# Optimization experiments

Measured on AMD Instinct MI355X. Metric: run time of the kernel, lower is better.

Reference implementation:

```python
import jax, jax.numpy as jnp
import numpy as np

N = 50000          # node_num
E = 800000         # edges before self-loops (avg degree 16)
H = 1              # heads
C = 64             # out_channel (== embedding dim)
D_IN = 64          # in_channel
NEG_SLOPE = 0.2    # GraphLayer leaky_relu negative_slope
BN_EPS = 1e-5


def setup_inputs() -> dict:
    key = jax.random.key(0)
    ks = jax.random.split(key, 12)
    x = jax.random.normal(ks[0], (N, D_IN), jnp.float32)
    # random edges with no self-loops (forward removes then re-adds self-loops)
    src = jax.random.randint(ks[1], (E,), 0, N, dtype=jnp.int32)
    off = jax.random.randint(ks[2], (E,), 1, N, dtype=jnp.int32)
    dst = (src + off) % N
    edge_index = jnp.stack([src, dst])            # [2, E], row0=j (source), row1=i (target)
    embedding = jax.random.normal(ks[3], (N, C), jnp.float32)
    sc = 1.0 / np.sqrt(D_IN)
    W = jax.random.normal(ks[4], (H * C, D_IN), jnp.float32) * sc   # lin.weight
    att_i = jax.random.normal(ks[5], (1, H, C), jnp.float32) * 0.1
    att_j = jax.random.normal(ks[6], (1, H, C), jnp.float32) * 0.1
    att_em_i = jax.random.normal(ks[7], (1, H, C), jnp.float32) * 0.1
    att_em_j = jax.random.normal(ks[8], (1, H, C), jnp.float32) * 0.1
    bias = jnp.zeros((C,), jnp.float32)           # GraphLayer bias (concat=False)
    bn_gamma = jnp.ones((C,), jnp.float32)
    bn_beta = jnp.zeros((C,), jnp.float32)
    return {"x": x, "edge_index": edge_index, "embedding": embedding, "W": W,
            "att_i": att_i, "att_j": att_j, "att_em_i": att_em_i, "att_em_j": att_em_j,
            "bias": bias, "bn_gamma": bn_gamma, "bn_beta": bn_beta}


def reference(x, edge_index, embedding, W, att_i, att_j, att_em_i, att_em_j, bias, bn_gamma, bn_beta):
    n = x.shape[0]
    xl = (x @ W.T).reshape(n, H, C)                       # lin(x) -> [N, H, C]
    # add self-loops (input edges have none)
    loops = jnp.arange(n, dtype=edge_index.dtype)
    src = jnp.concatenate([edge_index[0], loops])         # j
    dst = jnp.concatenate([edge_index[1], loops])         # i (aggregation target)
    x_j = xl[src]                                         # [E', H, C]
    x_i = xl[dst]
    emb_i = embedding[dst][:, None, :]                    # [E', 1, C] broadcast over heads
    emb_j = embedding[src][:, None, :]
    # alpha = <cat(x_i, emb_i), cat(att_i, att_em_i)> + <cat(x_j, emb_j), cat(att_j, att_em_j)>
    a = ((x_i * att_i).sum(-1) + (emb_i * att_em_i).sum(-1)
         + (x_j * att_j).sum(-1) + (emb_j * att_em_j).sum(-1))   # [E', H]
    a = jnp.where(a >= 0, a, NEG_SLOPE * a)               # leaky_relu(0.2)
    # segment softmax over target nodes
    amax = jax.ops.segment_max(a, dst, num_segments=n)    # every node has a self-loop
    ea = jnp.exp(a - amax[dst])
    denom = jax.ops.segment_sum(ea, dst, num_segments=n)
    alpha = ea / (denom[dst] + 1e-16)                     # [E', H]
    msg = x_j * alpha[..., None]                          # [E', H, C]
    out = jax.ops.segment_sum(msg, dst, num_segments=n)   # [N, H, C]
    out = out.mean(axis=1) + bias                         # concat=False -> head mean
    # BatchNorm1d (training mode: batch stats) + ReLU
    mu = out.mean(axis=0)
    var = ((out - mu) ** 2).mean(axis=0)
    out = (out - mu) * jax.lax.rsqrt(var + BN_EPS) * bn_gamma + bn_beta
    return jnp.maximum(out, 0.0)
```

## Files before the change

kernel.cpp:

```cpp
#include <hip/hip_runtime.h>
#include <hip/hip_bf16.h>

#define NEG_SLOPE 0.2f
#define BN_EPS 1e-5f
#define CAP 48
#define OWNMAX 768

typedef __attribute__((ext_vector_type(8))) short bf16x8;
typedef __attribute__((ext_vector_type(4))) float f32x4;

__device__ __forceinline__ bf16x8 pk8(float4 a, float4 b) {
    union { __hip_bfloat16 h; short s; } u;
    bf16x8 r;
    u.h = __float2bfloat16(a.x); r[0] = u.s;
    u.h = __float2bfloat16(a.y); r[1] = u.s;
    u.h = __float2bfloat16(a.z); r[2] = u.s;
    u.h = __float2bfloat16(a.w); r[3] = u.s;
    u.h = __float2bfloat16(b.x); r[4] = u.s;
    u.h = __float2bfloat16(b.y); r[5] = u.s;
    u.h = __float2bfloat16(b.z); r[6] = u.s;
    u.h = __float2bfloat16(b.w); r[7] = u.s;
    return r;
}

__global__ void __launch_bounds__(256, 8)
k_scatter_mfma(const float* __restrict__ x, const float* __restrict__ W,
               const float* __restrict__ emb,
               const float* __restrict__ att_i, const float* __restrict__ att_j,
               const float* __restrict__ att_em_i, const float* __restrict__ att_em_j,
               const int* __restrict__ src, const int* __restrict__ dst, int E,
               int* __restrict__ cursor, unsigned short* __restrict__ bucket,
               __hip_bfloat16* __restrict__ xlh, float* __restrict__ s_i,
               float* __restrict__ s_j, int N) {
    __shared__ int nown;
    __shared__ int ownidx[OWNMAX];
    __shared__ int owndst[OWNMAX];
    int tid = threadIdx.x;
    {
        int myx = blockIdx.x & 7;
        int slice = blockIdx.x >> 3;
        int per = ((E + 255) >> 8);
        per = (per + 3) & ~3;
        int e0 = slice * per;
        int e1 = e0 + per; if (e1 > E) e1 = E;
        if (tid == 0) nown = 0;
        __syncthreads();
        if (e0 < e1) {
            int e1a = e0 + ((e1 - e0) & ~3);
#define APP(dd, ee) if ((((dd) >> 6) & 7) == myx) { \
            int k_ = atomicAdd(&nown, 1); \
            if (k_ < OWNMAX) { ownidx[k_] = (ee); owndst[k_] = (dd); } }
            for (int e = e0 + tid * 4; e < e1a; e += 1024) {
                int4 d4 = *(const int4*)(dst + e);
                APP(d4.x, e)
                APP(d4.y, e + 1)
                APP(d4.z, e + 2)
                APP(d4.w, e + 3)
            }
            for (int e = e1a + tid; e < e1; e += 256) {
                int d = dst[e];
                APP(d, e)
            }
#undef APP
        }
        __syncthreads();
        int n = nown < OWNMAX ? nown : OWNMAX;
        int k0 = tid, k1 = tid + 256;
        bool v0 = k0 < n, v1 = k1 < n;
        int ea = v0 ? ownidx[k0] : 0, da = v0 ? owndst[k0] : 0;
        int eb = v1 ? ownidx[k1] : 0, db = v1 ? owndst[k1] : 0;
        int sa = v0 ? src[ea] : 0;
        int sb = v1 ? src[eb] : 0;
        if (v0) {
            int p = atomicAdd(&cursor[da], 1);
            if (p < CAP) bucket[(size_t)da * CAP + p] = (unsigned short)sa;
        }
        if (v1) {
            int p = atomicAdd(&cursor[db], 1);
            if (p < CAP) bucket[(size_t)db * CAP + p] = (unsigned short)sb;
        }
        for (int k = tid + 512; k < n; k += 256) {
            int e = ownidx[k];
            int d = owndst[k];
            int p = atomicAdd(&cursor[d], 1);
            if (p < CAP) bucket[(size_t)d * CAP + p] = (unsigned short)src[e];
        }
    }

    int gw = blockIdx.x * 4 + (tid >> 6);
    int ntiles = (N + 15) >> 4;
    if (gw >= ntiles) return;
    int lane = tid & 63;
    int m = lane & 15;
    int q = lane >> 4;
    int r0 = gw * 16;

    const float* xrow = x + (size_t)(r0 + m) * 64;
    float4 xa0 = *(const float4*)(xrow + q * 8);
    float4 xa1 = *(const float4*)(xrow + q * 8 + 4);
    float4 xb0 = *(const float4*)(xrow + 32 + q * 8);
    float4 xb1 = *(const float4*)(xrow + 32 + q * 8 + 4);
    bf16x8 A0 = pk8(xa0, xa1);
    bf16x8 A1 = pk8(xb0, xb1);

    f32x4 acc0 = {0.f, 0.f, 0.f, 0.f}, acc1 = acc0, acc2 = acc0, acc3 = acc0;
#define CTILE(ct, accv) { \
        const float* wrow = W + (size_t)(ct * 16 + m) * 64; \
        float4 wb0 = *(const float4*)(wrow + q * 8); \
        float4 wb1 = *(const float4*)(wrow + q * 8 + 4); \
        float4 wb2 = *(const float4*)(wrow + 32 + q * 8); \
        float4 wb3 = *(const float4*)(wrow + 32 + q * 8 + 4); \
        bf16x8 B0 = pk8(wb0, wb1); \
        bf16x8 B1 = pk8(wb2, wb3); \
        accv = __builtin_amdgcn_mfma_f32_16x16x32_bf16(A0, B0, accv, 0, 0, 0); \
        accv = __builtin_amdgcn_mfma_f32_16x16x32_bf16(A1, B1, accv, 0, 0, 0); }
    CTILE(0, acc0) CTILE(1, acc1) CTILE(2, acc2) CTILE(3, acc3)
#undef CTILE

    float ati0 = att_i[m],    ati1 = att_i[16 + m],    ati2 = att_i[32 + m],    ati3 = att_i[48 + m];
    float atj0 = att_j[m],    atj1 = att_j[16 + m],    atj2 = att_j[32 + m],    atj3 = att_j[48 + m];
    float aei0 = att_em_i[m], aei1 = att_em_i[16 + m], aei2 = att_em_i[32 + m], aei3 = att_em_i[48 + m];
    float aej0 = att_em_j[m], aej1 = att_em_j[16 + m], aej2 = att_em_j[32 + m], aej3 = att_em_j[48 + m];
#pragma unroll
    for (int reg = 0; reg < 4; ++reg) {
        int r = r0 + q * 4 + reg;
        if (r < N) {
            float v0 = acc0[reg], v1 = acc1[reg], v2 = acc2[reg], v3 = acc3[reg];
            __hip_bfloat16* xo = xlh + (size_t)r * 64 + m;
            xo[0]  = __float2bfloat16(v0);
            xo[16] = __float2bfloat16(v1);
            xo[32] = __float2bfloat16(v2);
            xo[48] = __float2bfloat16(v3);
            const float* er = emb + (size_t)r * 64 + m;
            float e0 = er[0], e1 = er[16], e2 = er[32], e3 = er[48];
            float pi = v0 * ati0 + v1 * ati1 + v2 * ati2 + v3 * ati3
                     + e0 * aei0 + e1 * aei1 + e2 * aei2 + e3 * aei3;
            float pj = v0 * atj0 + v1 * atj1 + v2 * atj2 + v3 * atj3
                     + e0 * aej0 + e1 * aej1 + e2 * aej2 + e3 * aej3;
#pragma unroll
            for (int o = 1; o < 16; o <<= 1) {
                pi += __shfl_xor(pi, o, 64);
                pj += __shfl_xor(pj, o, 64);
            }
            if (m == 0) { s_i[r] = pi; s_j[r] = pj; }
        }
    }
}

__global__ void __launch_bounds__(256, 8)
k_aggregate(const __hip_bfloat16* __restrict__ xlh, const float* __restrict__ s_i,
            const float* __restrict__ s_j, const int* __restrict__ cursor,
            const unsigned short* __restrict__ bucket, const float* __restrict__ bias,
            __hip_bfloat16* __restrict__ preh, int N) {
    int lane = threadIdx.x & 63;
    int w = threadIdx.x >> 6;
    int blk = blockIdx.x;
    int t = blk >> 3;
    int g = ((t >> 4) << 7) + ((blk & 7) << 4) + (t & 15);
    int i = g * 4 + w;
    if (i >= N) return;

    int deg = cursor[i];
    deg = deg < CAP ? deg : CAP;
    size_t base = (size_t)i * CAP;
    float sii = s_i[i];
    float sji = s_j[i];
    float selfx = (float)xlh[(size_t)i * 64 + lane];
    float bi = bias[lane];
    int jreg = 0;
    if (lane < deg) jreg = (int)bucket[base + lane];
    float areg = -1e30f;
    if (lane < deg) {
        float a = sii + s_j[jreg];
        areg = a >= 0.f ? a : NEG_SLOPE * a;
    }
    float a_self = sii + sji;
    a_self = a_self >= 0.f ? a_self : NEG_SLOPE * a_self;
    float mx = fmaxf(a_self, areg);
#pragma unroll
    for (int o = 32; o; o >>= 1) mx = fmaxf(mx, __shfl_xor(mx, o, 64));
    float wreg = (lane < deg) ? __expf(areg - mx) : 0.f;
    float dsum = wreg;
#pragma unroll
    for (int o = 32; o; o >>= 1) dsum += __shfl_xor(dsum, o, 64);
    float w_self = __expf(a_self - mx);
    float denom = dsum + w_self + 1e-16f;

    float acc = w_self * selfx;
    int wbits = __float_as_int(wreg);
    int nb = (deg + 15) >> 4;
#define GL(k) int j##k = __builtin_amdgcn_readlane(jreg, e + k); \
              float u##k = __int_as_float(__builtin_amdgcn_readlane(wbits, e + k)); \
              float v##k = (float)xlh[(size_t)j##k * 64 + lane];
#define FM(k) acc = fmaf(u##k, v##k, acc);
    for (int b = 0; b < nb; ++b) {
        int e = b << 4;
        GL(0) GL(1) GL(2) GL(3) GL(4) GL(5) GL(6) GL(7)
        GL(8) GL(9) GL(10) GL(11) GL(12) GL(13) GL(14) GL(15)
        FM(0) FM(1) FM(2) FM(3) FM(4) FM(5) FM(6) FM(7)
        FM(8) FM(9) FM(10) FM(11) FM(12) FM(13) FM(14) FM(15)
    }
#undef GL
#undef FM
    preh[(size_t)i * 64 + lane] = __float2bfloat16(acc / denom + bi);
}

__global__ void k_stats(const __hip_bfloat16* __restrict__ preh, int N,
                        float* __restrict__ sums) {
    int lane = threadIdx.x & 63, w = threadIdx.x >> 6;
    int gwave = blockIdx.x * (blockDim.x >> 6) + w;
    int stride = gridDim.x * (blockDim.x >> 6);
    float s = 0.f, q = 0.f;
    for (int r = gwave; r < N; r += stride) {
        float v = (float)preh[(size_t)r * 64 + lane];
        s += v;
        q = fmaf(v, v, q);
    }
    __shared__ float ls[4][64], lq[4][64];
    ls[w][lane] = s;
    lq[w][lane] = q;
    __syncthreads();
    if (w == 0) {
        s = ls[0][lane] + ls[1][lane] + ls[2][lane] + ls[3][lane];
        q = lq[0][lane] + lq[1][lane] + lq[2][lane] + lq[3][lane];
        atomicAdd(&sums[lane], s);
        atomicAdd(&sums[64 + lane], q);
    }
}

__global__ void __launch_bounds__(256, 4)
k_norm(const __hip_bfloat16* __restrict__ preh, const float* __restrict__ sums,
       const float* __restrict__ gamma, const float* __restrict__ beta,
       float* __restrict__ out, int N, int total4) {
    __shared__ float sc_sh[64], sh_sh[64];
    int tid = threadIdx.x;
    if (tid < 64) {
        float invN = 1.f / (float)N;
        float mu = sums[tid] * invN;
        float var = sums[64 + tid] * invN - mu * mu;
        float sc = gamma[tid] * rsqrtf(var + BN_EPS);
        sc_sh[tid] = sc;
        sh_sh[tid] = beta[tid] - mu * sc;
    }
    __syncthreads();
    typedef __attribute__((ext_vector_type(4))) short s16x4;
    union { s16x4 v; short s[4]; } u;
    for (int i = blockIdx.x * blockDim.x + tid; i < total4; i += gridDim.x * blockDim.x) {
        int c = (i & 15) * 4;
        u.v = ((const s16x4*)preh)[i];
        float4 r;
        union { __hip_bfloat16 h; short s; } cv;
        cv.s = u.s[0]; r.x = fmaxf(fmaf((float)cv.h, sc_sh[c + 0], sh_sh[c + 0]), 0.f);
        cv.s = u.s[1]; r.y = fmaxf(fmaf((float)cv.h, sc_sh[c + 1], sh_sh[c + 1]), 0.f);
        cv.s = u.s[2]; r.z = fmaxf(fmaf((float)cv.h, sc_sh[c + 2], sh_sh[c + 2]), 0.f);
        cv.s = u.s[3]; r.w = fmaxf(fmaf((float)cv.h, sc_sh[c + 3], sh_sh[c + 3]), 0.f);
        ((float4*)out)[i] = r;
    }
}

extern "C" void kernel_launch(void* const* d_in, const int* in_sizes, int n_in,
                              void* d_out, int out_size, void* d_ws, size_t ws_size,
                              hipStream_t stream) {
    const float* x        = (const float*)d_in[0];
    const int*   ei       = (const int*)d_in[1];
    const float* emb      = (const float*)d_in[2];
    const float* W        = (const float*)d_in[3];
    const float* att_i    = (const float*)d_in[4];
    const float* att_j    = (const float*)d_in[5];
    const float* att_em_i = (const float*)d_in[6];
    const float* att_em_j = (const float*)d_in[7];
    const float* bias     = (const float*)d_in[8];
    const float* gamma    = (const float*)d_in[9];
    const float* beta     = (const float*)d_in[10];

    int N = in_sizes[0] / 64;
    int E = in_sizes[1] / 2;
    const int* srcv = ei;
    const int* dstv = ei + E;

    char* ws = (char*)d_ws;
    size_t o = 0;
    auto alloc = [&](size_t bytes) -> char* {
        char* p = ws + o;
        o += bytes;
        o = (o + 255) & ~(size_t)255;
        return p;
    };
    __hip_bfloat16* xlh    = (__hip_bfloat16*)alloc((size_t)N * 64 * 2);
    __hip_bfloat16* preh   = (__hip_bfloat16*)alloc((size_t)N * 64 * 2);
    float* s_i             = (float*)alloc((size_t)N * 4);
    float* s_j             = (float*)alloc((size_t)N * 4);
    unsigned short* bucket = (unsigned short*)alloc((size_t)N * CAP * 2);
    char*  zbase  = alloc((size_t)N * 4 + 128 * 4);
    int*   cursor = (int*)zbase;
    float* sums   = (float*)(zbase + (size_t)N * 4);

    hipMemsetAsync(zbase, 0, (size_t)N * 4 + 128 * 4, stream);

    k_scatter_mfma<<<2048, 256, 0, stream>>>(x, W, emb, att_i, att_j, att_em_i,
                                             att_em_j, srcv, dstv, E, cursor, bucket,
                                             xlh, s_i, s_j, N);
    int nblk2 = (((N + 3) / 4) + 127) & ~127;
    k_aggregate<<<nblk2, 256, 0, stream>>>(xlh, s_i, s_j, cursor, bucket,
                                           bias, preh, N);
    k_stats<<<256, 256, 0, stream>>>(preh, N, sums);
    int total4 = N * 16;
    k_norm<<<512, 256, 0, stream>>>(preh, sums, gamma, beta, (float*)d_out, N, total4);
}
```

Baseline: 179.7 us.

## Fuse BN stats into aggregate, pack src/dst in LDS, hoist x loads

The scatter kernel now reads src alongside dst and packs both as 16-bit halves into one LDS word. This removes the dependent global src[e] gather in the bucket-fill phase and halves LDS usage. The x-row loads for the MFMA tile are issued before the scatter phase so their latency overlaps it. The aggregate kernel becomes a persistent grid-stride loop over a fixed 2048-block grid with XCD-aware node mapping, and it accumulates BatchNorm sums directly, which eliminates the separate k_stats kernel and its re-read of preh. The packing assumes node indices fit in 16 bits, the same assumption the existing bucket storage already makes.

Result: slower. 204.6 us (+13.9%).

```diff
diff --git a/kernel.cpp b/kernel.cpp
--- a/kernel.cpp
+++ b/kernel.cpp
@@ -33,9 +33,22 @@
                __hip_bfloat16* __restrict__ xlh, float* __restrict__ s_i,
                float* __restrict__ s_j, int N) {
     __shared__ int nown;
-    __shared__ int ownidx[OWNMAX];
-    __shared__ int owndst[OWNMAX];
+    __shared__ unsigned int own[OWNMAX];
     int tid = threadIdx.x;
+
+    int gw = blockIdx.x * 4 + (tid >> 6);
+    int ntiles = (N + 15) >> 4;
+    int lane = tid & 63;
+    int m = lane & 15;
+    int q = lane >> 4;
+    int r0 = gw * 16;
+    int rload = r0 + m; if (rload > N - 1) rload = N - 1;
+    const float* xrow = x + (size_t)rload * 64;
+    float4 xa0 = *(const float4*)(xrow + q * 8);
+    float4 xa1 = *(const float4*)(xrow + q * 8 + 4);
+    float4 xb0 = *(const float4*)(xrow + 32 + q * 8);
+    float4 xb1 = *(const float4*)(xrow + 32 + q * 8 + 4);
+
     {
         int myx = blockIdx.x & 7;
         int slice = blockIdx.x >> 3;
@@ -47,59 +60,46 @@
         __syncthreads();
         if (e0 < e1) {
             int e1a = e0 + ((e1 - e0) & ~3);
-#define APP(dd, ee) if ((((dd) >> 6) & 7) == myx) { \
+#define APP(dd, ss) if ((((dd) >> 6) & 7) == myx) { \
             int k_ = atomicAdd(&nown, 1); \
-            if (k_ < OWNMAX) { ownidx[k_] = (ee); owndst[k_] = (dd); } }
+            if (k_ < OWNMAX) own[k_] = ((unsigned)(dd) << 16) | (unsigned)(ss); }
             for (int e = e0 + tid * 4; e < e1a; e += 1024) {
                 int4 d4 = *(const int4*)(dst + e);
-                APP(d4.x, e)
-                APP(d4.y, e + 1)
-                APP(d4.z, e + 2)
-                APP(d4.w, e + 3)
+                int4 s4 = *(const int4*)(src + e);
+                APP(d4.x, s4.x)
+                APP(d4.y, s4.y)
+                APP(d4.z, s4.z)
+                APP(d4.w, s4.w)
             }
             for (int e = e1a + tid; e < e1; e += 256) {
-                int d = dst[e];
-                APP(d, e)
+                int d = dst[e]; int s = src[e];
+                APP(d, s)
             }
 #undef APP
         }
         __syncthreads();
         int n = nown < OWNMAX ? nown : OWNMAX;
-        int k0 = tid, k1 = tid + 256;
-        bool v0 = k0 < n, v1 = k1 < n;
-        int ea = v0 ? ownidx[k0] : 0, da = v0 ? owndst[k0] : 0;
-        int eb = v1 ? ownidx[k1] : 0, db = v1 ? owndst[k1] : 0;
-        int sa = v0 ? src[ea] : 0;
-        int sb = v1 ? src[eb] : 0;
-        if (v0) {
-            int p = atomicAdd(&cursor[da], 1);
-            if (p < CAP) bucket[(size_t)da * CAP + p] = (unsigned short)sa;
-        }
-        if (v1) {
-            int p = atomicAdd(&cursor[db], 1);
-            if (p < CAP) bucket[(size_t)db * CAP + p] = (unsigned short)sb;
+        unsigned pa = (tid < n) ? own[tid] : 0u;
+        unsigned pb = (tid + 256 < n) ? own[tid + 256] : 0u;
+        if (tid < n) {
+            int d = pa >> 16;
+            int p = atomicAdd(&cursor[d], 1);
+            if (p < CAP) bucket[(size_t)d * CAP + p] = (unsigned short)(pa & 0xffffu);
+        }
+        if (tid + 256 < n) {
+            int d = pb >> 16;
+            int p = atomicAdd(&cursor[d], 1);
+            if (p < CAP) bucket[(size_t)d * CAP + p] = (unsigned short)(pb & 0xffffu);
         }
         for (int k = tid + 512; k < n; k += 256) {
-            int e = ownidx[k];
-            int d = owndst[k];
+            unsigned pc = own[k];
+            int d = pc >> 16;
             int p = atomicAdd(&cursor[d], 1);
-            if (p < CAP) bucket[(size_t)d * CAP + p] = (unsigned short)src[e];
-        }
-    }
-
-    int gw = blockIdx.x * 4 + (tid >> 6);
-    int ntiles = (N + 15) >> 4;
+            if (p < CAP) bucket[(size_t)d * CAP + p] = (unsigned short)(pc & 0xffffu);
+        }
+    }
+
     if (gw >= ntiles) return;
-    int lane = tid & 63;
-    int m = lane & 15;
-    int q = lane >> 4;
-    int r0 = gw * 16;
-
-    const float* xrow = x + (size_t)(r0 + m) * 64;
-    float4 xa0 = *(const float4*)(xrow + q * 8);
-    float4 xa1 = *(const float4*)(xrow + q * 8 + 4);
-    float4 xb0 = *(const float4*)(xrow + 32 + q * 8);
-    float4 xb1 = *(const float4*)(xrow + 32 + q * 8 + 4);
     bf16x8 A0 = pk8(xa0, xa1);
     bf16x8 A1 = pk8(xb0, xb1);
 
@@ -151,80 +151,73 @@
 k_aggregate(const __hip_bfloat16* __restrict__ xlh, const float* __restrict__ s_i,
             const float* __restrict__ s_j, const int* __restrict__ cursor,
             const unsigned short* __restrict__ bucket, const float* __restrict__ bias,
-            __hip_bfloat16* __restrict__ preh, int N) {
+            __hip_bfloat16* __restrict__ preh, float* __restrict__ sums, int N) {
     int lane = threadIdx.x & 63;
     int w = threadIdx.x >> 6;
-    int blk = blockIdx.x;
-    int t = blk >> 3;
-    int g = ((t >> 4) << 7) + ((blk & 7) << 4) + (t & 15);
-    int i = g * 4 + w;
-    if (i >= N) return;
-
-    int deg = cursor[i];
-    deg = deg < CAP ? deg : CAP;
-    size_t base = (size_t)i * CAP;
-    float sii = s_i[i];
-    float sji = s_j[i];
-    float selfx = (float)xlh[(size_t)i * 64 + lane];
+    int xg = blockIdx.x & 7;
+    int t = blockIdx.x >> 3;
     float bi = bias[lane];
-    int jreg = 0;
-    if (lane < deg) jreg = (int)bucket[base + lane];
-    float areg = -1e30f;
-    if (lane < deg) {
-        float a = sii + s_j[jreg];
-        areg = a >= 0.f ? a : NEG_SLOPE * a;
-    }
-    float a_self = sii + sji;
-    a_self = a_self >= 0.f ? a_self : NEG_SLOPE * a_self;
-    float mx = fmaxf(a_self, areg);
+    float bs = 0.f, bq = 0.f;
+    int nmax = ((N + 511) >> 9) << 6;
+    for (int n = t * 4 + w; n < nmax; n += 1024) {
+        int i = ((n >> 6) << 9) | (xg << 6) | (n & 63);
+        if (i < N) {
+            int deg = cursor[i];
+            deg = deg < CAP ? deg : CAP;
+            size_t base = (size_t)i * CAP;
+            float sii = s_i[i];
+            float sji = s_j[i];
+            float selfx = (float)xlh[(size_t)i * 64 + lane];
+            int jreg = 0;
+            if (lane < deg) jreg = (int)bucket[base + lane];
+            float areg = -1e30f;
+            if (lane < deg) {
+                float a = sii + s_j[jreg];
+                areg = a >= 0.f ? a : NEG_SLOPE * a;
+            }
+            float a_self = sii + sji;
+            a_self = a_self >= 0.f ? a_self : NEG_SLOPE * a_self;
+            float mx = fmaxf(a_self, areg);
 #pragma unroll
-    for (int o = 32; o; o >>= 1) mx = fmaxf(mx, __shfl_xor(mx, o, 64));
-    float wreg = (lane < deg) ? __expf(areg - mx) : 0.f;
-    float dsum = wreg;
+            for (int o = 32; o; o >>= 1) mx = fmaxf(mx, __shfl_xor(mx, o, 64));
+            float wreg = (lane < deg) ? __expf(areg - mx) : 0.f;
+            float dsum = wreg;
 #pragma unroll
-    for (int o = 32; o; o >>= 1) dsum += __shfl_xor(dsum, o, 64);
-    float w_self = __expf(a_self - mx);
-    float denom = dsum + w_self + 1e-16f;
-
-    float acc = w_self * selfx;
-    int wbits = __float_as_int(wreg);
-    int nb = (deg + 15) >> 4;
+            for (int o = 32; o; o >>= 1) dsum += __shfl_xor(dsum, o, 64);
+            float w_self = __expf(a_self - mx);
+            float denom = dsum + w_self + 1e-16f;
+
+            float acc = w_self * selfx;
+            int wbits = __float_as_int(wreg);
+            int nb = (deg + 15) >> 4;
 #define GL(k) int j##k = __builtin_amdgcn_readlane(jreg, e + k); \
               float u##k = __int_as_float(__builtin_amdgcn_readlane(wbits, e + k)); \
               float v##k = (float)xlh[(size_t)j##k * 64 + lane];
 #define FM(k) acc = fmaf(u##k, v##k, acc);
-    for (int b = 0; b < nb; ++b) {
-        int e = b << 4;
-        GL(0) GL(1) GL(2) GL(3) GL(4) GL(5) GL(6) GL(7)
-        GL(8) GL(9) GL(10) GL(11) GL(12) GL(13) GL(14) GL(15)
-        FM(0) FM(1) FM(2) FM(3) FM(4) FM(5) FM(6) FM(7)
-        FM(8) FM(9) FM(10) FM(11) FM(12) FM(13) FM(14) FM(15)
-    }
+            for (int b = 0; b < nb; ++b) {
+                int e = b << 4;
+                GL(0) GL(1) GL(2) GL(3) GL(4) GL(5) GL(6) GL(7)
+                GL(8) GL(9) GL(10) GL(11) GL(12) GL(13) GL(14) GL(15)
+                FM(0) FM(1) FM(2) FM(3) FM(4) FM(5) FM(6) FM(7)
+                FM(8) FM(9) FM(10) FM(11) FM(12) FM(13) FM(14) FM(15)
+            }
 #undef GL
 #undef FM
-    preh[(size_t)i * 64 + lane] = __float2bfloat16(acc / denom + bi);
-}
-
-__global__ void k_stats(const __hip_bfloat16* __restrict__ preh, int N,
-                        float* __restrict__ sums) {
-    int lane = threadIdx.x & 63, w = threadIdx.x >> 6;
-    int gwave = blockIdx.x * (blockDim.x >> 6) + w;
-    int stride = gridDim.x * (blockDim.x >> 6);
-    float s = 0.f, q = 0.f;
-    for (int r = gwave; r < N; r += stride) {
-        float v = (float)preh[(size_t)r * 64 + lane];
-        s += v;
-        q = fmaf(v, v, q);
+            float v = acc / denom + bi;
+            preh[(size_t)i * 64 + lane] = __float2bfloat16(v);
+            bs += v;
+            bq = fmaf(v, v, bq);
+        }
     }
     __shared__ float ls[4][64], lq[4][64];
-    ls[w][lane] = s;
-    lq[w][lane] = q;
+    ls[w][lane] = bs;
+    lq[w][lane] = bq;
     __syncthreads();
     if (w == 0) {
-        s = ls[0][lane] + ls[1][lane] + ls[2][lane] + ls[3][lane];
-        q = lq[0][lane] + lq[1][lane] + lq[2][lane] + lq[3][lane];
+        float s = ls[0][lane] + ls[1][lane] + ls[2][lane] + ls[3][lane];
+        float qq = lq[0][lane] + lq[1][lane] + lq[2][lane] + lq[3][lane];
         atomicAdd(&sums[lane], s);
-        atomicAdd(&sums[64 + lane], q);
+        atomicAdd(&sums[64 + lane], qq);
     }
 }
 
@@ -300,10 +293,8 @@
     k_scatter_mfma<<<2048, 256, 0, stream>>>(x, W, emb, att_i, att_j, att_em_i,
                                              att_em_j, srcv, dstv, E, cursor, bucket,
                                              xlh, s_i, s_j, N);
-    int nblk2 = (((N + 3) / 4) + 127) & ~127;
-    k_aggregate<<<nblk2, 256, 0, stream>>>(xlh, s_i, s_j, cursor, bucket,
-                                           bias, preh, N);
-    k_stats<<<256, 256, 0, stream>>>(preh, N, sums);
+    k_aggregate<<<2048, 256, 0, stream>>>(xlh, s_i, s_j, cursor, bucket,
+                                          bias, preh, sums, N);
     int total4 = N * 16;
     k_norm<<<512, 256, 0, stream>>>(preh, sums, gamma, beta, (float*)d_out, N, total4);
 }
```
